# Optimization experiments

Measured on AMD Instinct MI355X. Metric: run time of the kernel, lower is better.

The kernel has to match this reference:

```python
import jax, jax.numpy as jnp
import numpy as np

EMBED_DIM = 1024
NUM_HEADS = 16
HEAD_DIM = EMBED_DIM // NUM_HEADS
BATCH = 4
SEQ = 2048


def setup_inputs() -> dict:
    key = jax.random.key(0)
    ks = jax.random.split(key, 9)
    s = 1.0 / np.sqrt(EMBED_DIM)
    return {
        "query": jax.random.normal(ks[0], (BATCH, SEQ, EMBED_DIM), jnp.float32),
        "Wq": jax.random.normal(ks[1], (EMBED_DIM, EMBED_DIM), jnp.float32) * s,
        "bq": jnp.zeros((EMBED_DIM,), jnp.float32),
        "Wk": jax.random.normal(ks[2], (EMBED_DIM, EMBED_DIM), jnp.float32) * s,
        "bk": jnp.zeros((EMBED_DIM,), jnp.float32),
        "Wv": jax.random.normal(ks[3], (EMBED_DIM, EMBED_DIM), jnp.float32) * s,
        "bv": jnp.zeros((EMBED_DIM,), jnp.float32),
        "Wo": jax.random.normal(ks[4], (EMBED_DIM, EMBED_DIM), jnp.float32) * s,
        "bo": jnp.zeros((EMBED_DIM,), jnp.float32),
    }


def reference(query, Wq, bq, Wk, bk, Wv, bv, Wo, bo):
    bsz, seq, embed_dim = query.shape
    scaling = HEAD_DIM ** (-0.5)
    # projections (torch Linear: x @ W.T + b)
    q = (query @ Wq.T + bq) * scaling
    k = query @ Wk.T + bk
    v = query @ Wv.T + bv
    # [b, h, s, d]
    q = q.reshape(bsz, seq, NUM_HEADS, HEAD_DIM).transpose(0, 2, 1, 3)
    k = k.reshape(bsz, seq, NUM_HEADS, HEAD_DIM).transpose(0, 2, 1, 3)
    v = v.reshape(bsz, seq, NUM_HEADS, HEAD_DIM).transpose(0, 2, 1, 3)
    # full [b, h, s, s] scores (faithful to the naive original)
    scores = jnp.einsum("bhqd,bhkd->bhqk", q, k)
    causal = jnp.tril(jnp.ones((seq, seq), bool))  # [s, s]
    scores = jnp.where(causal[None, None], scores, -jnp.inf)
    probs = jax.nn.softmax(scores, axis=-1)
    attn = jnp.einsum("bhqk,bhkd->bhqd", probs, v)
    attn = attn.transpose(0, 2, 1, 3).reshape(bsz, seq, embed_dim)
    return attn @ Wo.T + bo
```

## Files before the change

### kernel.cpp

```cpp
#include <hip/hip_runtime.h>
#include <stdint.h>

typedef unsigned short u16;
typedef __attribute__((ext_vector_type(8))) __bf16 bf16x8;
typedef __attribute__((ext_vector_type(4))) float f32x4;

#define SEQL 2048
#define NHEADS 16
#define HDIM 64
#define BSZ 4
#define EMB 1024
#define MROWS (BSZ * SEQL)
#define LOG2E 1.44269504088896f

__device__ __forceinline__ u16 f2bf(float f) {
  union { float f; uint32_t u; } v; v.f = f;
  return (u16)((v.u + 0x7fffu + ((v.u >> 16) & 1u)) >> 16);
}

__device__ __forceinline__ void gload_lds16(const u16* g, u16* l) {
  __builtin_amdgcn_global_load_lds(
      (__attribute__((address_space(1))) void*)(g),
      (__attribute__((address_space(3))) void*)(l), 16, 0, 0);
}

__device__ __forceinline__ void cvt8(const float* __restrict__ in, u16* __restrict__ out, int i) {
  float4 a = *(const float4*)(in + i);
  float4 b = *(const float4*)(in + i + 4);
  uint4 o;
  o.x = f2bf(a.x) | ((uint32_t)f2bf(a.y) << 16);
  o.y = f2bf(a.z) | ((uint32_t)f2bf(a.w) << 16);
  o.z = f2bf(b.x) | ((uint32_t)f2bf(b.y) << 16);
  o.w = f2bf(b.z) | ((uint32_t)f2bf(b.w) << 16);
  *(uint4*)(out + i) = o;
}

#define XN (MROWS * EMB)
__global__ void cvt_all(const float* __restrict__ query,
                        const float* __restrict__ w0, const float* __restrict__ w1,
                        const float* __restrict__ w2, const float* __restrict__ w3,
                        u16* __restrict__ Xb, u16* __restrict__ Wqb) {
  int i = (blockIdx.x * blockDim.x + threadIdx.x) * 8;
  if (i < XN) {
    cvt8(query, Xb, i);
  } else {
    int j = i - XN;
    int w = j >> 20;
    int jj = j & 1048575;
    const float* src = w == 0 ? w0 : w == 1 ? w1 : w == 2 ? w2 : w3;
    cvt8(src, Wqb + ((size_t)w << 20), jj);
  }
}

__device__ __forceinline__ void gemm_core(const u16* __restrict__ A, const u16* __restrict__ B,
                                          int m0, int n0, u16* As, u16* Bs, f32x4 acc[4][4]) {
  const int tid = threadIdx.x;
  const int lane = tid & 63;
  const int wid = tid >> 6;
  const int wm = wid >> 1, wn = wid & 1;
  const int srow = lane >> 2;
  const int scol = (lane & 3) * 8;
  const int lrow = lane & 15;
  const int kg = (lane >> 4) * 8;

  const u16* Ag0 = A + (size_t)(m0 + wid * 32 + srow) * EMB + scol;
  const u16* Bg0 = B + (size_t)(n0 + wid * 32 + srow) * EMB + scol;
  u16* Al0 = As + (wid * 32 + srow) * 32 + scol;
  u16* Bl0 = Bs + (wid * 32 + srow) * 32 + scol;

  for (int k0 = 0; k0 < EMB; k0 += 32) {
    gload_lds16(Ag0 + k0, Al0);
    gload_lds16(Ag0 + k0 + 16 * EMB, Al0 + 16 * 32);
    gload_lds16(Bg0 + k0, Bl0);
    gload_lds16(Bg0 + k0 + 16 * EMB, Bl0 + 16 * 32);
    __syncthreads();
    bf16x8 af[4], bfr[4];
#pragma unroll
    for (int f = 0; f < 4; ++f) {
      af[f]  = *(const bf16x8*)(As + (wm * 64 + f * 16 + lrow) * 32 + kg);
      bfr[f] = *(const bf16x8*)(Bs + (wn * 64 + f * 16 + lrow) * 32 + kg);
    }
#pragma unroll
    for (int fm = 0; fm < 4; ++fm)
#pragma unroll
      for (int fn = 0; fn < 4; ++fn)
        acc[fm][fn] = __builtin_amdgcn_mfma_f32_16x16x32_bf16(af[fm], bfr[fn], acc[fm][fn], 0, 0, 0);
    __syncthreads();
  }
}

__global__ __launch_bounds__(256, 2) void gemm_qkv(
    const u16* __restrict__ X,
    const u16* __restrict__ Wq, const u16* __restrict__ Wk, const u16* __restrict__ Wv,
    const float* __restrict__ bq, const float* __restrict__ bk, const float* __restrict__ bv,
    u16* __restrict__ Qb, u16* __restrict__ Kb, u16* __restrict__ Vt) {
  __shared__ u16 As[128 * 32];
  __shared__ u16 Bs[128 * 32];
  const int which = blockIdx.y;
  const u16* W = which == 0 ? Wq : which == 1 ? Wk : Wv;
  const float* bias = which == 0 ? bq : which == 1 ? bk : bv;

  const int mt = blockIdx.x >> 3, nt = blockIdx.x & 7;
  const f32x4 fzero = {0.f, 0.f, 0.f, 0.f};
  f32x4 acc[4][4];
#pragma unroll
  for (int i = 0; i < 4; ++i)
#pragma unroll
    for (int j = 0; j < 4; ++j) acc[i][j] = fzero;

  gemm_core(X, W, mt * 128, nt * 128, As, Bs, acc);

  const int lane = threadIdx.x & 63;
  const int wid = threadIdx.x >> 6;
  const int wm = wid >> 1, wn = wid & 1;
  const int lrow = lane & 15, g = lane >> 4;

  if (which == 2) {
#pragma unroll
    for (int fm = 0; fm < 4; ++fm)
#pragma unroll
      for (int fn = 0; fn < 4; ++fn) {
        int n = nt * 128 + wn * 64 + fn * 16 + lrow;
        float bs = bias[n];
        int h = n >> 6, d = n & 63;
        int m0 = mt * 128 + wm * 64 + fm * 16 + g * 4;
        int b = m0 >> 11, s = m0 & 2047;
        union { u16 s4[4]; uint2 u; } o;
#pragma unroll
        for (int r = 0; r < 4; ++r) o.s4[r] = f2bf(acc[fm][fn][r] + bs);
        *(uint2*)(Vt + ((size_t)(b * NHEADS + h) * HDIM + d) * SEQL + s) = o.u;
      }
  } else {
    u16* Ob = which == 0 ? Qb : Kb;
    const float scale = which == 0 ? 0.125f * LOG2E : 1.0f;
#pragma unroll
    for (int fm = 0; fm < 4; ++fm)
#pragma unroll
      for (int fn = 0; fn < 4; ++fn) {
        int n = nt * 128 + wn * 64 + fn * 16 + lrow;
        float bs = bias[n];
        int h = n >> 6, d = n & 63;
#pragma unroll
        for (int r = 0; r < 4; ++r) {
          int m = mt * 128 + wm * 64 + fm * 16 + g * 4 + r;
          int b = m >> 11, s = m & 2047;
          float v = (acc[fm][fn][r] + bs) * scale;
          Ob[(size_t)((b * NHEADS + h) * SEQL + s) * HDIM + d] = f2bf(v);
        }
      }
  }
}

__global__ __launch_bounds__(256, 2) void gemm_out(
    const u16* __restrict__ Ain, const u16* __restrict__ Wo,
    const float* __restrict__ bo, float* __restrict__ out) {
  __shared__ u16 As[128 * 32];
  __shared__ u16 Bs[128 * 32];
  const int mt = blockIdx.x >> 3, nt = blockIdx.x & 7;
  const f32x4 fzero = {0.f, 0.f, 0.f, 0.f};
  f32x4 acc[4][4];
#pragma unroll
  for (int i = 0; i < 4; ++i)
#pragma unroll
    for (int j = 0; j < 4; ++j) acc[i][j] = fzero;

  gemm_core(Ain, Wo, mt * 128, nt * 128, As, Bs, acc);

  const int lane = threadIdx.x & 63;
  const int wid = threadIdx.x >> 6;
  const int wm = wid >> 1, wn = wid & 1;
  const int lrow = lane & 15, g = lane >> 4;
#pragma unroll
  for (int fm = 0; fm < 4; ++fm)
#pragma unroll
    for (int fn = 0; fn < 4; ++fn) {
      int n = nt * 128 + wn * 64 + fn * 16 + lrow;
      float bs = bo[n];
#pragma unroll
      for (int r = 0; r < 4; ++r) {
        int m = mt * 128 + wm * 64 + fm * 16 + g * 4 + r;
        out[(size_t)m * EMB + n] = acc[fm][fn][r] + bs;
      }
    }
}

__device__ __forceinline__ int swz(int row, int colE) {
  return row * 64 + (colE ^ ((row & 7) << 3));
}

__global__ __launch_bounds__(256, 4) void attn4_kernel(
    const u16* __restrict__ Qb, const u16* __restrict__ Kb, const u16* __restrict__ Vt,
    u16* __restrict__ Ab) {
  __shared__ u16 Ks[2][64 * 64];
  __shared__ u16 Vs[2][64 * 64];

  const int bid = blockIdx.x;
  const int qa  = bid >> 6;
  const int bh  = bid & 63;

  const int tid = threadIdx.x, lane = tid & 63, wid = tid >> 6;
  const int lrow = lane & 15, g = lane >> 4, kg = g * 8;

  const u16* Qbh = Qb + (size_t)bh * SEQL * HDIM;
  const u16* Kbh = Kb + (size_t)bh * SEQL * HDIM;
  const u16* Vbh = Vt + (size_t)bh * HDIM * SEQL;

  const int srow = tid >> 3;
  const int sce  = (tid & 7) * 8;

  const f32x4 fzero = {0.f, 0.f, 0.f, 0.f};
  const int b = bh >> 4, h = bh & 15;

#pragma unroll 1
  for (int ph = 0; ph < 2; ++ph) {
    const int qt = ph ? (31 - qa) : qa;
    const int q0 = qt * 64;
    const int NT = qt + 1;

    const int qrow = q0 + wid * 16 + lrow;
    const bf16x8 qf0 = *(const bf16x8*)(Qbh + (size_t)qrow * HDIM + kg);
    const bf16x8 qf1 = *(const bf16x8*)(Qbh + (size_t)qrow * HDIM + 32 + kg);

    float m_run = -1e30f, l_run = 0.f;
    f32x4 accO[4];
#pragma unroll
    for (int d = 0; d < 4; ++d) accO[d] = fzero;

    {
      uint4 k0 = *(const uint4*)(Kbh + (size_t)srow * HDIM + sce);
      uint4 k1 = *(const uint4*)(Kbh + (size_t)(srow + 32) * HDIM + sce);
      uint4 v0 = *(const uint4*)(Vbh + (size_t)srow * SEQL + sce);
      uint4 v1 = *(const uint4*)(Vbh + (size_t)(srow + 32) * SEQL + sce);
      *(uint4*)(&Ks[0][swz(srow, sce)]) = k0;
      *(uint4*)(&Ks[0][swz(srow + 32, sce)]) = k1;
      *(uint4*)(&Vs[0][swz(srow, sce)]) = v0;
      *(uint4*)(&Vs[0][swz(srow + 32, sce)]) = v1;
    }
    __syncthreads();

    for (int t = 0; t < NT; ++t) {
      const int cur = t & 1;
      const int kv0 = t * 64;
      const bool pf = (t + 1 < NT);
      uint4 k0, k1, v0, v1;
      if (pf) {
        const int kvn = kv0 + 64;
        k0 = *(const uint4*)(Kbh + (size_t)(kvn + srow) * HDIM + sce);
        k1 = *(const uint4*)(Kbh + (size_t)(kvn + srow + 32) * HDIM + sce);
        v0 = *(const uint4*)(Vbh + (size_t)srow * SEQL + kvn + sce);
        v1 = *(const uint4*)(Vbh + (size_t)(srow + 32) * SEQL + kvn + sce);
      }

      f32x4 sacc[4];
      __builtin_amdgcn_s_setprio(1);
#pragma unroll
      for (int kb = 0; kb < 4; ++kb) {
        bf16x8 kfa = *(const bf16x8*)(&Ks[cur][swz(kb * 16 + lrow, kg)]);
        bf16x8 kfb = *(const bf16x8*)(&Ks[cur][swz(kb * 16 + lrow, 32 + kg)]);
        f32x4 z = fzero;
        z = __builtin_amdgcn_mfma_f32_16x16x32_bf16(kfa, qf0, z, 0, 0, 0);
        z = __builtin_amdgcn_mfma_f32_16x16x32_bf16(kfb, qf1, z, 0, 0, 0);
        sacc[kb] = z;
      }
      __builtin_amdgcn_s_setprio(0);

      if (kv0 + 63 > q0 + wid * 16) {
#pragma unroll
        for (int kb = 0; kb < 4; ++kb)
#pragma unroll
          for (int r = 0; r < 4; ++r)
            if (kv0 + kb * 16 + g * 4 + r > qrow) sacc[kb][r] = -1e30f;
      }

      float mx = sacc[0][0];
#pragma unroll
      for (int kb = 0; kb < 4; ++kb)
#pragma unroll
        for (int r = 0; r < 4; ++r) mx = fmaxf(mx, sacc[kb][r]);
      mx = fmaxf(mx, __shfl_xor(mx, 16));
      mx = fmaxf(mx, __shfl_xor(mx, 32));

      if (!__all(mx <= m_run + 8.f)) {
        const float mnew = fmaxf(m_run, mx);
        const float sc = __builtin_amdgcn_exp2f(m_run - mnew);
        m_run = mnew;
        l_run *= sc;
#pragma unroll
        for (int d = 0; d < 4; ++d) accO[d] *= sc;
      }

      bf16x8 pa[2];
      float ls = 0.f;
#pragma unroll
      for (int kb = 0; kb < 4; ++kb)
#pragma unroll
        for (int r = 0; r < 4; ++r) {
          float p = __builtin_amdgcn_exp2f(sacc[kb][r] - m_run);
          ls += p;
          pa[kb >> 1][(kb & 1) * 4 + r] = (__bf16)p;
        }
      l_run += ls;

      __builtin_amdgcn_s_setprio(1);
#pragma unroll
      for (int ks = 0; ks < 2; ++ks)
#pragma unroll
        for (int d = 0; d < 4; ++d) {
          union { ushort4 h[2]; bf16x8 v; } vf;
          vf.h[0] = *(const ushort4*)(&Vs[cur][swz(d * 16 + lrow, ks * 32 + g * 4)]);
          vf.h[1] = *(const ushort4*)(&Vs[cur][swz(d * 16 + lrow, ks * 32 + 16 + g * 4)]);
          accO[d] = __builtin_amdgcn_mfma_f32_16x16x32_bf16(vf.v, pa[ks], accO[d], 0, 0, 0);
        }
      __builtin_amdgcn_s_setprio(0);

      if (pf) {
        const int nb = cur ^ 1;
        *(uint4*)(&Ks[nb][swz(srow, sce)]) = k0;
        *(uint4*)(&Ks[nb][swz(srow + 32, sce)]) = k1;
        *(uint4*)(&Vs[nb][swz(srow, sce)]) = v0;
        *(uint4*)(&Vs[nb][swz(srow + 32, sce)]) = v1;
      }
      __syncthreads();
    }

    float l = l_run;
    l += __shfl_xor(l, 16);
    l += __shfl_xor(l, 32);
    const float inv = 1.f / l;
#pragma unroll
    for (int d = 0; d < 4; ++d) {
      union { u16 s4[4]; uint2 u; } o;
#pragma unroll
      for (int r = 0; r < 4; ++r) o.s4[r] = f2bf(accO[d][r] * inv);
      *(uint2*)(Ab + (size_t)(b * SEQL + qrow) * EMB + h * HDIM + d * 16 + g * 4) = o.u;
    }
    __syncthreads();
  }
}

extern "C" void kernel_launch(void* const* d_in, const int* in_sizes, int n_in,
                              void* d_out, int out_size, void* d_ws, size_t ws_size,
                              hipStream_t stream) {
  (void)in_sizes; (void)n_in; (void)out_size; (void)ws_size;
  const float* query = (const float*)d_in[0];
  const float* Wq = (const float*)d_in[1];
  const float* bq = (const float*)d_in[2];
  const float* Wk = (const float*)d_in[3];
  const float* bk = (const float*)d_in[4];
  const float* Wv = (const float*)d_in[5];
  const float* bv = (const float*)d_in[6];
  const float* Wo = (const float*)d_in[7];
  const float* bo = (const float*)d_in[8];
  float* out = (float*)d_out;

  const size_t MB = 1u << 20;
  char* ws = (char*)d_ws;
  u16* Xb  = (u16*)(ws);
  u16* Wqb = (u16*)(ws + 16 * MB);
  u16* Wkb = (u16*)(ws + 18 * MB);
  u16* Wvb = (u16*)(ws + 20 * MB);
  u16* Wob = (u16*)(ws + 22 * MB);
  u16* Qbf = (u16*)(ws + 24 * MB);
  u16* Kbf = (u16*)(ws + 40 * MB);
  u16* Vtg = (u16*)(ws + 56 * MB);
  u16* Ab  = Xb;

  cvt_all<<<6144, 256, 0, stream>>>(query, Wq, Wk, Wv, Wo, Xb, Wqb);
  gemm_qkv<<<dim3(512, 3), 256, 0, stream>>>(Xb, Wqb, Wkb, Wvb, bq, bk, bv, Qbf, Kbf, Vtg);
  attn4_kernel<<<1024, 256, 0, stream>>>(Qbf, Kbf, Vtg, Ab);
  gemm_out<<<512, 256, 0, stream>>>(Ab, Wob, bo, out);
}
```

Measured before the change: 181.5 us.

## Rewrite projection GEMMs with 4-stage LDS pipeline, 128x256 tiles and fused QKV

Replaces the single-buffered GEMM core with a 4-stage global-to-LDS prefetch pipeline that uses explicit vmcnt waits and one barrier per k-step. It also widens tiles to 128x256 with 512 threads and treats the contiguous Wq/Wk/Wv buffers as one concatenated weight matrix. Block IDs are remapped for L2 locality. The aim is to hide global load latency and cut barrier and launch overhead in the QKV and output projections, at the cost of 96KB LDS per block, which limits occupancy.

```diff
diff --git a/kernel.cpp b/kernel.cpp
--- a/kernel.cpp
+++ b/kernel.cpp
@@ -12,13 +12,14 @@
 #define EMB 1024
 #define MROWS (BSZ * SEQL)
 #define LOG2E 1.44269504088896f
+#define NKT 32
 
 __device__ __forceinline__ u16 f2bf(float f) {
   union { float f; uint32_t u; } v; v.f = f;
   return (u16)((v.u + 0x7fffu + ((v.u >> 16) & 1u)) >> 16);
 }
 
-__device__ __forceinline__ void gload_lds16(const u16* g, u16* l) {
+__device__ __forceinline__ void g2l(const u16* g, u16* l) {
   __builtin_amdgcn_global_load_lds(
       (__attribute__((address_space(1))) void*)(g),
       (__attribute__((address_space(3))) void*)(l), 16, 0, 0);
@@ -52,55 +53,73 @@
   }
 }
 
-__device__ __forceinline__ void gemm_core(const u16* __restrict__ A, const u16* __restrict__ B,
-                                          int m0, int n0, u16* As, u16* Bs, f32x4 acc[4][4]) {
+#define GBODY(WSTR, KT, DOPF)                                                       \
+  {                                                                                 \
+    asm volatile("s_waitcnt " WSTR ::: "memory");                                   \
+    __builtin_amdgcn_sched_barrier(0);                                              \
+    __builtin_amdgcn_s_barrier();                                                   \
+    __builtin_amdgcn_sched_barrier(0);                                              \
+    if (DOPF) {                                                                     \
+      const int kp = (KT) + 3;                                                      \
+      u16* d = lds + (kp & 3) * 12288;                                              \
+      g2l(Agb + kp * 32, d + tid * 8);                                              \
+      g2l(Bgb0 + kp * 32, d + 4096 + tid * 8);                                      \
+      g2l(Bgb1 + kp * 32, d + 8192 + tid * 8);                                      \
+    }                                                                               \
+    const u16* Ab = lds + ((KT) & 3) * 12288;                                       \
+    const u16* Bb = Ab + 4096;                                                      \
+    bf16x8 af[4], bfr[4];                                                           \
+    _Pragma("unroll") for (int i = 0; i < 4; ++i) {                                 \
+      af[i] = *(const bf16x8*)(Ab + (wr * 64 + i * 16 + lrow) * 32 + kg);           \
+      bfr[i] = *(const bf16x8*)(Bb + (wc * 64 + i * 16 + lrow) * 32 + kg);          \
+    }                                                                               \
+    __builtin_amdgcn_s_setprio(1);                                                  \
+    _Pragma("unroll") for (int mi = 0; mi < 4; ++mi)                                \
+      _Pragma("unroll") for (int ni = 0; ni < 4; ++ni)                              \
+        acc[mi][ni] =                                                               \
+            __builtin_amdgcn_mfma_f32_16x16x32_bf16(af[mi], bfr[ni], acc[mi][ni],   \
+                                                    0, 0, 0);                       \
+    __builtin_amdgcn_s_setprio(0);                                                  \
+  }
+
+__device__ __forceinline__ void gemm_core256(const u16* __restrict__ A,
+                                             const u16* __restrict__ B,
+                                             int m0, int n0, u16* lds,
+                                             f32x4 acc[4][4]) {
   const int tid = threadIdx.x;
-  const int lane = tid & 63;
-  const int wid = tid >> 6;
-  const int wm = wid >> 1, wn = wid & 1;
-  const int srow = lane >> 2;
-  const int scol = (lane & 3) * 8;
-  const int lrow = lane & 15;
-  const int kg = (lane >> 4) * 8;
-
-  const u16* Ag0 = A + (size_t)(m0 + wid * 32 + srow) * EMB + scol;
-  const u16* Bg0 = B + (size_t)(n0 + wid * 32 + srow) * EMB + scol;
-  u16* Al0 = As + (wid * 32 + srow) * 32 + scol;
-  u16* Bl0 = Bs + (wid * 32 + srow) * 32 + scol;
-
-  for (int k0 = 0; k0 < EMB; k0 += 32) {
-    gload_lds16(Ag0 + k0, Al0);
-    gload_lds16(Ag0 + k0 + 16 * EMB, Al0 + 16 * 32);
-    gload_lds16(Bg0 + k0, Bl0);
-    gload_lds16(Bg0 + k0 + 16 * EMB, Bl0 + 16 * 32);
-    __syncthreads();
-    bf16x8 af[4], bfr[4];
-#pragma unroll
-    for (int f = 0; f < 4; ++f) {
-      af[f]  = *(const bf16x8*)(As + (wm * 64 + f * 16 + lrow) * 32 + kg);
-      bfr[f] = *(const bf16x8*)(Bs + (wn * 64 + f * 16 + lrow) * 32 + kg);
-    }
-#pragma unroll
-    for (int fm = 0; fm < 4; ++fm)
-#pragma unroll
-      for (int fn = 0; fn < 4; ++fn)
-        acc[fm][fn] = __builtin_amdgcn_mfma_f32_16x16x32_bf16(af[fm], bfr[fn], acc[fm][fn], 0, 0, 0);
-    __syncthreads();
-  }
-}
-
-__global__ __launch_bounds__(256, 2) void gemm_qkv(
-    const u16* __restrict__ X,
-    const u16* __restrict__ Wq, const u16* __restrict__ Wk, const u16* __restrict__ Wv,
+  const int lane = tid & 63, wid = tid >> 6;
+  const int wr = wid >> 2, wc = wid & 3;
+  const int lrow = lane & 15, kg = (lane >> 4) * 8;
+  const int srow = tid >> 2, scolE = (tid & 3) * 8;
+
+  const u16* Agb  = A + (size_t)(m0 + srow) * EMB + scolE;
+  const u16* Bgb0 = B + (size_t)(n0 + srow) * EMB + scolE;
+  const u16* Bgb1 = B + (size_t)(n0 + 128 + srow) * EMB + scolE;
+
+#pragma unroll
+  for (int t = 0; t < 3; ++t) {
+    u16* d = lds + t * 12288;
+    g2l(Agb + t * 32, d + tid * 8);
+    g2l(Bgb0 + t * 32, d + 4096 + tid * 8);
+    g2l(Bgb1 + t * 32, d + 8192 + tid * 8);
+  }
+
+#pragma unroll 1
+  for (int kt = 0; kt < NKT - 3; ++kt) GBODY("vmcnt(6)", kt, true)
+  GBODY("vmcnt(6)", NKT - 3, false)
+  GBODY("vmcnt(3)", NKT - 2, false)
+  GBODY("vmcnt(0)", NKT - 1, false)
+}
+
+__global__ __launch_bounds__(512, 2) void gemm_qkv3(
+    const u16* __restrict__ X, const u16* __restrict__ Wcat,
     const float* __restrict__ bq, const float* __restrict__ bk, const float* __restrict__ bv,
     u16* __restrict__ Qb, u16* __restrict__ Kb, u16* __restrict__ Vt) {
-  __shared__ u16 As[128 * 32];
-  __shared__ u16 Bs[128 * 32];
-  const int which = blockIdx.y;
-  const u16* W = which == 0 ? Wq : which == 1 ? Wk : Wv;
-  const float* bias = which == 0 ? bq : which == 1 ? bk : bv;
-
-  const int mt = blockIdx.x >> 3, nt = blockIdx.x & 7;
+  __shared__ u16 lds[4 * 12288];
+  const int orig = blockIdx.x;
+  const int virt = (orig & 7) * 96 + (orig >> 3);
+  const int mt = virt / 12, nt = virt % 12;
+
   const f32x4 fzero = {0.f, 0.f, 0.f, 0.f};
   f32x4 acc[4][4];
 #pragma unroll
@@ -108,55 +127,60 @@
 #pragma unroll
     for (int j = 0; j < 4; ++j) acc[i][j] = fzero;
 
-  gemm_core(X, W, mt * 128, nt * 128, As, Bs, acc);
-
-  const int lane = threadIdx.x & 63;
-  const int wid = threadIdx.x >> 6;
-  const int wm = wid >> 1, wn = wid & 1;
+  gemm_core256(X, Wcat, mt * 128, nt * 256, lds, acc);
+
+  const int tid = threadIdx.x, lane = tid & 63, wid = tid >> 6;
+  const int wr = wid >> 2, wc = wid & 3;
   const int lrow = lane & 15, g = lane >> 4;
+  const int which = nt >> 2;
+  const float* bias = which == 0 ? bq : which == 1 ? bk : bv;
+  const float scale = which == 0 ? 0.125f * LOG2E : 1.0f;
 
   if (which == 2) {
 #pragma unroll
-    for (int fm = 0; fm < 4; ++fm)
-#pragma unroll
-      for (int fn = 0; fn < 4; ++fn) {
-        int n = nt * 128 + wn * 64 + fn * 16 + lrow;
-        float bs = bias[n];
-        int h = n >> 6, d = n & 63;
-        int m0 = mt * 128 + wm * 64 + fm * 16 + g * 4;
-        int b = m0 >> 11, s = m0 & 2047;
+    for (int mi = 0; mi < 4; ++mi)
+#pragma unroll
+      for (int ni = 0; ni < 4; ++ni) {
+        int n = nt * 256 + wc * 64 + ni * 16 + lrow;
+        int nn = n & 1023;
+        float bs = bias[nn];
+        int h = nn >> 6, d = nn & 63;
+        int m0r = mt * 128 + wr * 64 + mi * 16 + g * 4;
+        int b = m0r >> 11, s = m0r & 2047;
         union { u16 s4[4]; uint2 u; } o;
 #pragma unroll
-        for (int r = 0; r < 4; ++r) o.s4[r] = f2bf(acc[fm][fn][r] + bs);
+        for (int r = 0; r < 4; ++r) o.s4[r] = f2bf(acc[mi][ni][r] + bs);
         *(uint2*)(Vt + ((size_t)(b * NHEADS + h) * HDIM + d) * SEQL + s) = o.u;
       }
   } else {
     u16* Ob = which == 0 ? Qb : Kb;
-    const float scale = which == 0 ? 0.125f * LOG2E : 1.0f;
-#pragma unroll
-    for (int fm = 0; fm < 4; ++fm)
-#pragma unroll
-      for (int fn = 0; fn < 4; ++fn) {
-        int n = nt * 128 + wn * 64 + fn * 16 + lrow;
-        float bs = bias[n];
-        int h = n >> 6, d = n & 63;
+#pragma unroll
+    for (int mi = 0; mi < 4; ++mi)
+#pragma unroll
+      for (int ni = 0; ni < 4; ++ni) {
+        int n = nt * 256 + wc * 64 + ni * 16 + lrow;
+        int nn = n & 1023;
+        float bs = bias[nn];
+        int h = nn >> 6, d = nn & 63;
 #pragma unroll
         for (int r = 0; r < 4; ++r) {
-          int m = mt * 128 + wm * 64 + fm * 16 + g * 4 + r;
+          int m = mt * 128 + wr * 64 + mi * 16 + g * 4 + r;
           int b = m >> 11, s = m & 2047;
-          float v = (acc[fm][fn][r] + bs) * scale;
+          float v = (acc[mi][ni][r] + bs) * scale;
           Ob[(size_t)((b * NHEADS + h) * SEQL + s) * HDIM + d] = f2bf(v);
         }
       }
   }
 }
 
-__global__ __launch_bounds__(256, 2) void gemm_out(
+__global__ __launch_bounds__(512, 2) void gemm_out2(
     const u16* __restrict__ Ain, const u16* __restrict__ Wo,
     const float* __restrict__ bo, float* __restrict__ out) {
-  __shared__ u16 As[128 * 32];
-  __shared__ u16 Bs[128 * 32];
-  const int mt = blockIdx.x >> 3, nt = blockIdx.x & 7;
+  __shared__ u16 lds[4 * 12288];
+  const int orig = blockIdx.x;
+  const int virt = (orig & 7) * 32 + (orig >> 3);
+  const int mt = virt >> 2, nt = virt & 3;
+
   const f32x4 fzero = {0.f, 0.f, 0.f, 0.f};
   f32x4 acc[4][4];
 #pragma unroll
@@ -164,22 +188,21 @@
 #pragma unroll
     for (int j = 0; j < 4; ++j) acc[i][j] = fzero;
 
-  gemm_core(Ain, Wo, mt * 128, nt * 128, As, Bs, acc);
-
-  const int lane = threadIdx.x & 63;
-  const int wid = threadIdx.x >> 6;
-  const int wm = wid >> 1, wn = wid & 1;
+  gemm_core256(Ain, Wo, mt * 128, nt * 256, lds, acc);
+
+  const int tid = threadIdx.x, lane = tid & 63, wid = tid >> 6;
+  const int wr = wid >> 2, wc = wid & 3;
   const int lrow = lane & 15, g = lane >> 4;
 #pragma unroll
-  for (int fm = 0; fm < 4; ++fm)
-#pragma unroll
-    for (int fn = 0; fn < 4; ++fn) {
-      int n = nt * 128 + wn * 64 + fn * 16 + lrow;
+  for (int mi = 0; mi < 4; ++mi)
+#pragma unroll
+    for (int ni = 0; ni < 4; ++ni) {
+      int n = nt * 256 + wc * 64 + ni * 16 + lrow;
       float bs = bo[n];
 #pragma unroll
       for (int r = 0; r < 4; ++r) {
-        int m = mt * 128 + wm * 64 + fm * 16 + g * 4 + r;
-        out[(size_t)m * EMB + n] = acc[fm][fn][r] + bs;
+        int m = mt * 128 + wr * 64 + mi * 16 + g * 4 + r;
+        out[(size_t)m * EMB + n] = acc[mi][ni][r] + bs;
       }
     }
 }
@@ -306,9 +329,9 @@
       for (int ks = 0; ks < 2; ++ks)
 #pragma unroll
         for (int d = 0; d < 4; ++d) {
-          union { ushort4 h[2]; bf16x8 v; } vf;
-          vf.h[0] = *(const ushort4*)(&Vs[cur][swz(d * 16 + lrow, ks * 32 + g * 4)]);
-          vf.h[1] = *(const ushort4*)(&Vs[cur][swz(d * 16 + lrow, ks * 32 + 16 + g * 4)]);
+          union { ushort4 h2[2]; bf16x8 v; } vf;
+          vf.h2[0] = *(const ushort4*)(&Vs[cur][swz(d * 16 + lrow, ks * 32 + g * 4)]);
+          vf.h2[1] = *(const ushort4*)(&Vs[cur][swz(d * 16 + lrow, ks * 32 + 16 + g * 4)]);
           accO[d] = __builtin_amdgcn_mfma_f32_16x16x32_bf16(vf.v, pa[ks], accO[d], 0, 0, 0);
         }
       __builtin_amdgcn_s_setprio(0);
@@ -357,8 +380,6 @@
   char* ws = (char*)d_ws;
   u16* Xb  = (u16*)(ws);
   u16* Wqb = (u16*)(ws + 16 * MB);
-  u16* Wkb = (u16*)(ws + 18 * MB);
-  u16* Wvb = (u16*)(ws + 20 * MB);
   u16* Wob = (u16*)(ws + 22 * MB);
   u16* Qbf = (u16*)(ws + 24 * MB);
   u16* Kbf = (u16*)(ws + 40 * MB);
@@ -366,7 +387,7 @@
   u16* Ab  = Xb;
 
   cvt_all<<<6144, 256, 0, stream>>>(query, Wq, Wk, Wv, Wo, Xb, Wqb);
-  gemm_qkv<<<dim3(512, 3), 256, 0, stream>>>(Xb, Wqb, Wkb, Wvb, bq, bk, bv, Qbf, Kbf, Vtg);
+  gemm_qkv3<<<768, 512, 0, stream>>>(Xb, Wqb, bq, bk, bv, Qbf, Kbf, Vtg);
   attn4_kernel<<<1024, 256, 0, stream>>>(Qbf, Kbf, Vtg, Ab);
-  gemm_out<<<512, 256, 0, stream>>>(Ab, Wob, bo, out);
-}
+  gemm_out2<<<256, 512, 0, stream>>>(Ab, Wob, bo, out);
+}
```

Measured after the change: 165.3 us. 1.1x faster.
